# Performance work log

Measured on AMD Instinct MI355X. Metric: run time of the kernel, lower is better.

The kernel has to match this reference:

```python
import jax, jax.numpy as jnp
import numpy as np

B, N, F, S, M, K = 32, 4096, 256, 256, 1024, 11
EPS = 1e-06  # slot-attention epsilon
LN_EPS = 1e-05  # torch LayerNorm default
NUM_ITERS = 3


def _ln(x, g, b):
    mu = jnp.mean(x, axis=-1, keepdims=True)
    var = jnp.mean(jnp.square(x - mu), axis=-1, keepdims=True)
    return (x - mu) * jax.lax.rsqrt(var + LN_EPS) * g + b


def setup_inputs() -> dict:
    key = jax.random.key(0)
    ks = jax.random.split(key, 12)
    def xavier(k, shape):
        fan_in, fan_out = shape[0], shape[-1]
        lim = np.sqrt(6.0 / (fan_in + fan_out))
        return jax.random.uniform(k, shape, jnp.float32, -lim, lim)
    return {
        "features": jax.random.normal(ks[0], (B, N, F), jnp.float32),
        "sigma": jnp.array([0.1], jnp.float32),
        "z": jax.random.normal(ks[1], (B, K, S), jnp.float32),
        "slots_init_w": xavier(ks[2], (K, S)),
        "gf": jnp.ones((F,), jnp.float32), "bf": jnp.zeros((F,), jnp.float32),
        "gs": jnp.ones((S,), jnp.float32), "bs": jnp.zeros((S,), jnp.float32),
        "gm": jnp.ones((S,), jnp.float32), "bm": jnp.zeros((S,), jnp.float32),
        "Wk": xavier(ks[3], (F, S)),
        "Wv": xavier(ks[4], (F, S)),
        "Wq": xavier(ks[5], (S, S)),
        "W_ih": xavier(ks[6], (3 * S, S)),
        "W_hh": xavier(ks[7], (3 * S, S)),
        "b_ih": jnp.zeros((3 * S,), jnp.float32),
        "b_hh": jnp.zeros((3 * S,), jnp.float32),
        "W1": xavier(ks[8], (S, M)), "b1": jnp.zeros((M,), jnp.float32),
        "W2": xavier(ks[9], (M, S)), "b2": jnp.zeros((S,), jnp.float32),
    }


def _gru(x, h, W_ih, W_hh, b_ih, b_hh):
    # torch GRUCell: gates ordered (r, z, n)
    gi = x @ W_ih.T + b_ih  # [..., 3S]
    gh = h @ W_hh.T + b_hh
    ir, iz, inn = jnp.split(gi, 3, axis=-1)
    hr, hz, hn = jnp.split(gh, 3, axis=-1)
    r = jax.nn.sigmoid(ir + hr)
    zg = jax.nn.sigmoid(iz + hz)
    n = jnp.tanh(inn + r * hn)
    return (1.0 - zg) * n + zg * h


def reference(features, sigma, z, slots_init_w, gf, bf, gs, bs, gm, bm,
              Wk, Wv, Wq, W_ih, W_hh, b_ih, b_hh, W1, b1, W2, b2):
    mu = jnp.broadcast_to(slots_init_w[None], (features.shape[0], K, S))
    slots_init = mu + z * sigma * jax.lax.stop_gradient(mu)
    feats = _ln(features, gf, bf)
    k = feats @ Wk  # [B,N,S]
    v = feats @ Wv  # [B,N,S]
    D = v.shape[-1]
    scale = D ** -0.5
    slots = slots_init
    attn = None
    for i in range(NUM_ITERS):
        if i == NUM_ITERS - 1:
            slots = jax.lax.stop_gradient(slots) + slots_init - jax.lax.stop_gradient(slots_init)
        slots_prev = slots
        q = _ln(slots, gs, bs) @ Wq  # [B,K,S]
        attn_logits = jnp.einsum('bid,bjd->bij', q, k) * scale  # [B,K,N]
        attn = jax.nn.softmax(attn_logits, axis=1)  # softmax over slots axis
        attn_wm = attn / (jnp.sum(attn, axis=-1, keepdims=True) + EPS)
        updates = jnp.einsum('bij,bjd->bid', attn_wm, v)  # [B,K,S]
        slots = _gru(updates, slots_prev, W_ih, W_hh, b_ih, b_hh)
        slots = slots + (jax.nn.relu(_ln(slots, gm, bm) @ W1 + b1) @ W2 + b2)
    return slots, attn
```

## Files before the change

### kernel.cpp

```cpp
#include <hip/hip_runtime.h>

#define EPS 1e-6f
#define LN_EPS 1e-5f

typedef unsigned short u16;
typedef unsigned int u32;
typedef short bf16x8 __attribute__((ext_vector_type(8)));
typedef float f32x4 __attribute__((ext_vector_type(4)));

__device__ __forceinline__ float bf2f(u16 u) {
  return __uint_as_float(((u32)u) << 16);
}
__device__ __forceinline__ u16 f2bf(float f) {
  u32 x = __float_as_uint(f);
  x += 0x7fffu + ((x >> 16) & 1u);
  return (u16)(x >> 16);
}

__global__ void init_slots_kernel(const float* __restrict__ w,
                                  const float* __restrict__ z,
                                  const float* __restrict__ sigma,
                                  float* __restrict__ slots,
                                  float* __restrict__ upd,
                                  float* __restrict__ sums) {
  int i = blockIdx.x * 256 + threadIdx.x;
  int s = i & 255;
  int k = (i >> 8) % 11;
  float wv = w[k * 256 + s];
  slots[i] = wv + z[i] * sigma[0] * wv;
  upd[i] = 0.f;
  if (i < 352) sums[i] = 0.f;
}

__global__ void wprep_kernel(const float* __restrict__ W_ih,
                             const float* __restrict__ W_hh,
                             const float* __restrict__ W1,
                             const float* __restrict__ W2,
                             const float* __restrict__ Wq,
                             const float* __restrict__ Wk,
                             const float* __restrict__ Wv,
                             float* __restrict__ wihT, float* __restrict__ whhT,
                             short* __restrict__ W1b, short* __restrict__ W2b,
                             short* __restrict__ Wqb, short* __restrict__ Btb) {
  int e = blockIdx.x * 256 + threadIdx.x;
  if (e < 196608) {
    int j = e >> 8, d = e & 255;
    wihT[d * 768 + j] = W_ih[e];
  } else if (e < 393216) {
    int e2 = e - 196608;
    int j = e2 >> 8, d = e2 & 255;
    whhT[d * 768 + j] = W_hh[e2];
  } else if (e < 655360) {
    int e2 = e - 393216;
    W1b[e2] = (short)f2bf(W1[e2]);
  } else if (e < 917504) {
    int e2 = e - 655360;
    W2b[e2] = (short)f2bf(W2[e2]);
  } else if (e < 983040) {
    int e2 = e - 917504;
    Wqb[e2] = (short)f2bf(Wq[e2]);
  } else if (e < 1114112) {
    int e2 = e - 983040;
    int f = e2 >> 9, j = e2 & 511;
    float v = (j < 256) ? Wk[f * 256 + j] : Wv[f * 256 + (j - 256)];
    Btb[j * 256 + f] = (short)f2bf(v);
  }
}

__global__ __launch_bounds__(256) void gemm_kv(
    const float* __restrict__ feat, const short* __restrict__ Btb,
    const float* __restrict__ gf, const float* __restrict__ bfp,
    short* __restrict__ kt, short* __restrict__ vbuf) {
  __shared__ short As[16384];
  __shared__ short Bs[2][8192];
  int t = threadIdx.x;
  int w = t >> 6, lane = t & 63;
  int quad = lane >> 4, l16 = lane & 15;
  int i0 = blockIdx.x * 64;
  int wi = (w & 1) * 32, wj = (w >> 1) * 64;

  {
    #pragma unroll
    for (int c = 0; c < 4; ++c) {
      int lin = c * 256 + t;
      int jr = lin >> 3, p = lin & 7;
      int q = (p - jr) & 7;
      const short* gB = Btb + (long)jr * 256 + q * 8;
      __builtin_amdgcn_global_load_lds(
          (const __attribute__((address_space(1))) void*)gB,
          (__attribute__((address_space(3))) void*)&Bs[0][lin * 8], 16, 0, 0);
    }
  }

  {
    int r = t >> 2;
    int qd = t & 3;
    const float* frow = feat + (long)(i0 + r) * 256 + qd * 64;
    float4 fv[16];
    float s = 0.f, s2 = 0.f;
    #pragma unroll
    for (int i = 0; i < 16; ++i) {
      fv[i] = *(const float4*)(frow + i * 4);
      s += fv[i].x + fv[i].y + fv[i].z + fv[i].w;
      s2 += fv[i].x * fv[i].x + fv[i].y * fv[i].y + fv[i].z * fv[i].z +
            fv[i].w * fv[i].w;
    }
    s += __shfl_xor(s, 1); s2 += __shfl_xor(s2, 1);
    s += __shfl_xor(s, 2); s2 += __shfl_xor(s2, 2);
    float mu = s * (1.f / 256.f);
    float rs = rsqrtf(s2 * (1.f / 256.f) - mu * mu + LN_EPS);
    #pragma unroll
    for (int c = 0; c < 8; ++c) {
      float4 a = fv[c * 2], b = fv[c * 2 + 1];
      int fb = qd * 64 + c * 8;
      float4 g0 = *(const float4*)(gf + fb);
      float4 g1 = *(const float4*)(gf + fb + 4);
      float4 e0 = *(const float4*)(bfp + fb);
      float4 e1 = *(const float4*)(bfp + fb + 4);
      bf16x8 pk;
      pk[0] = (short)f2bf((a.x - mu) * rs * g0.x + e0.x);
      pk[1] = (short)f2bf((a.y - mu) * rs * g0.y + e0.y);
      pk[2] = (short)f2bf((a.z - mu) * rs * g0.z + e0.z);
      pk[3] = (short)f2bf((a.w - mu) * rs * g0.w + e0.w);
      pk[4] = (short)f2bf((b.x - mu) * rs * g1.x + e1.x);
      pk[5] = (short)f2bf((b.y - mu) * rs * g1.y + e1.y);
      pk[6] = (short)f2bf((b.z - mu) * rs * g1.z + e1.z);
      pk[7] = (short)f2bf((b.w - mu) * rs * g1.w + e1.w);
      int p = qd * 8 + ((c + 2 * qd + r) & 7);
      *(bf16x8*)&As[r * 256 + p * 8] = pk;
    }
  }
  __syncthreads();

  f32x4 acc[2][4];
  #pragma unroll
  for (int a = 0; a < 2; ++a)
    #pragma unroll
    for (int b = 0; b < 4; ++b) acc[a][b] = (f32x4){0.f, 0.f, 0.f, 0.f};

  for (int idx = 0; idx < 16; ++idx) {
    int jq = idx >> 2, ks = idx & 3;
    int buf = idx & 1;
    if (idx < 15) {
      int jn = (idx + 1) >> 2, kn = (idx + 1) & 3;
      #pragma unroll
      for (int c = 0; c < 4; ++c) {
        int lin = c * 256 + t;
        int jr = lin >> 3, p = lin & 7;
        int q = (p - jr) & 7;
        const short* gB = Btb + (long)(jn * 128 + jr) * 256 + kn * 64 + q * 8;
        __builtin_amdgcn_global_load_lds(
            (const __attribute__((address_space(1))) void*)gB,
            (__attribute__((address_space(3))) void*)&Bs[buf ^ 1][lin * 8],
            16, 0, 0);
      }
    }
    #pragma unroll
    for (int kh = 0; kh < 2; ++kh) {
      bf16x8 af[2], bfr[4];
      #pragma unroll
      for (int mi = 0; mi < 2; ++mi) {
        int m = wi + mi * 16 + l16;
        int p = ks * 8 + ((kh * 4 + quad + 2 * ks + m) & 7);
        af[mi] = *(const bf16x8*)&As[m * 256 + p * 8];
      }
      #pragma unroll
      for (int ni = 0; ni < 4; ++ni) {
        int j = wj + ni * 16 + l16;
        int p = ((kh * 4 + quad) + j) & 7;
        bfr[ni] = *(const bf16x8*)&Bs[buf][j * 64 + p * 8];
      }
      if (jq < 2) {
        #pragma unroll
        for (int mi = 0; mi < 2; ++mi)
          #pragma unroll
          for (int ni = 0; ni < 4; ++ni)
            acc[mi][ni] = __builtin_amdgcn_mfma_f32_16x16x32_bf16(
                af[mi], bfr[ni], acc[mi][ni], 0, 0, 0);
      } else {
        #pragma unroll
        for (int mi = 0; mi < 2; ++mi)
          #pragma unroll
          for (int ni = 0; ni < 4; ++ni)
            acc[mi][ni] = __builtin_amdgcn_mfma_f32_16x16x32_bf16(
                bfr[ni], af[mi], acc[mi][ni], 0, 0, 0);
      }
    }
    if (ks == 3) {
      if (jq < 2) {
        #pragma unroll
        for (int ni = 0; ni < 4; ++ni) {
          int j = jq * 128 + wj + ni * 16 + l16;
          #pragma unroll
          for (int mi = 0; mi < 2; ++mi) {
            long ib = i0 + wi + mi * 16 + quad * 4;
            ushort4 u;
            u.x = f2bf(acc[mi][ni][0]);
            u.y = f2bf(acc[mi][ni][1]);
            u.z = f2bf(acc[mi][ni][2]);
            u.w = f2bf(acc[mi][ni][3]);
            *(ushort4*)&kt[(long)j * 131072 + ib] = u;
          }
        }
      } else {
        #pragma unroll
        for (int mi = 0; mi < 2; ++mi) {
          long i = i0 + wi + mi * 16 + l16;
          #pragma unroll
          for (int ni = 0; ni < 4; ++ni) {
            int sb = (jq - 2) * 128 + wj + ni * 16 + quad * 4;
            ushort4 u;
            u.x = f2bf(acc[mi][ni][0]);
            u.y = f2bf(acc[mi][ni][1]);
            u.z = f2bf(acc[mi][ni][2]);
            u.w = f2bf(acc[mi][ni][3]);
            *(ushort4*)&vbuf[i * 256 + sb] = u;
          }
        }
      }
      #pragma unroll
      for (int a = 0; a < 2; ++a)
        #pragma unroll
        for (int b = 0; b < 4; ++b) acc[a][b] = (f32x4){0.f, 0.f, 0.f, 0.f};
    }
    __syncthreads();
  }
}

__global__ __launch_bounds__(256) void qproj_kernel(
    const float* __restrict__ slots, const float* __restrict__ gs,
    const float* __restrict__ bs, const short* __restrict__ Wqb,
    float* __restrict__ qout) {
  __shared__ float lnq[256];
  __shared__ float red[8];
  int row = blockIdx.x, t = threadIdx.x;
  int w = t >> 6, lane = t & 63;
  float x = slots[(long)row * 256 + t];
  float s = x, s2 = x * x;
  #pragma unroll
  for (int off = 32; off > 0; off >>= 1) {
    s += __shfl_xor(s, off);
    s2 += __shfl_xor(s2, off);
  }
  if (lane == 0) { red[w * 2] = s; red[w * 2 + 1] = s2; }
  __syncthreads();
  float st = red[0] + red[2] + red[4] + red[6];
  float st2 = red[1] + red[3] + red[5] + red[7];
  float mu = st * (1.f / 256.f);
  float rs = rsqrtf(st2 * (1.f / 256.f) - mu * mu + LN_EPS);
  lnq[t] = (x - mu) * rs * gs[t] + bs[t];
  __syncthreads();
  float acc = 0.f;
  for (int k = 0; k < 256; ++k)
    acc += lnq[k] * bf2f((u16)Wqb[k * 256 + t]);
  qout[(long)row * 256 + t] = acc;
}

__global__ __launch_bounds__(256) void attn_upd(
    const float* __restrict__ q, const short* __restrict__ kt,
    const short* __restrict__ vb, float* __restrict__ attn_out,
    float* __restrict__ sums, float* __restrict__ upd, int emit_attn) {
  __shared__ float qs[3072];
  __shared__ float ps[11 * 512];
  int b = blockIdx.y;
  int n0 = blockIdx.x * 512;
  int t = threadIdx.x, lane = t & 63;
  for (int e = t; e < 2816; e += 256) {
    int kk = e >> 8, f = e & 255;
    qs[f * 12 + kk] = q[b * 2816 + e];
  }
  __syncthreads();
  long base = (long)b * 4096 + n0 + 2 * t;
  float a0[11], a1[11];
  #pragma unroll
  for (int kk = 0; kk < 11; ++kk) { a0[kk] = 0.f; a1[kk] = 0.f; }
  for (int f = 0; f < 256; ++f) {
    u32 u = *(const u32*)(kt + (long)f * 131072 + base);
    float k0 = bf2f((u16)(u & 0xffffu));
    float k1 = bf2f((u16)(u >> 16));
    float4 qa = *(const float4*)&qs[f * 12];
    float4 qb4 = *(const float4*)&qs[f * 12 + 4];
    float4 qc = *(const float4*)&qs[f * 12 + 8];
    a0[0] += k0 * qa.x;  a1[0] += k1 * qa.x;
    a0[1] += k0 * qa.y;  a1[1] += k1 * qa.y;
    a0[2] += k0 * qa.z;  a1[2] += k1 * qa.z;
    a0[3] += k0 * qa.w;  a1[3] += k1 * qa.w;
    a0[4] += k0 * qb4.x; a1[4] += k1 * qb4.x;
    a0[5] += k0 * qb4.y; a1[5] += k1 * qb4.y;
    a0[6] += k0 * qb4.z; a1[6] += k1 * qb4.z;
    a0[7] += k0 * qb4.w; a1[7] += k1 * qb4.w;
    a0[8] += k0 * qc.x;  a1[8] += k1 * qc.x;
    a0[9] += k0 * qc.y;  a1[9] += k1 * qc.y;
    a0[10] += k0 * qc.z; a1[10] += k1 * qc.z;
  }
  float m0 = -1e30f, m1 = -1e30f;
  #pragma unroll
  for (int kk = 0; kk < 11; ++kk) {
    a0[kk] *= 0.0625f;
    a1[kk] *= 0.0625f;
    m0 = fmaxf(m0, a0[kk]);
    m1 = fmaxf(m1, a1[kk]);
  }
  float s0 = 0.f, s1 = 0.f;
  #pragma unroll
  for (int kk = 0; kk < 11; ++kk) {
    a0[kk] = expf(a0[kk] - m0);
    a1[kk] = expf(a1[kk] - m1);
    s0 += a0[kk];
    s1 += a1[kk];
  }
  float i0 = 1.0f / s0, i1 = 1.0f / s1;
  #pragma unroll
  for (int kk = 0; kk < 11; ++kk) {
    float p0 = a0[kk] * i0, p1 = a1[kk] * i1;
    *(float2*)&ps[kk * 512 + 2 * t] = make_float2(p0, p1);
    if (emit_attn)
      *(float2*)(attn_out + ((long)b * 11 + kk) * 4096 + n0 + 2 * t) =
          make_float2(p0, p1);
    float sv = p0 + p1;
    #pragma unroll
    for (int off = 32; off > 0; off >>= 1) sv += __shfl_xor(sv, off);
    if (lane == 0) atomicAdd(&sums[b * 11 + kk], sv);
  }
  __syncthreads();
  int sp = t & 127, nh = t >> 7;
  float2 acc[11];
  #pragma unroll
  for (int kk = 0; kk < 11; ++kk) acc[kk] = make_float2(0.f, 0.f);
  const u32* vb2 =
      (const u32*)(vb + ((long)b * 4096 + n0 + nh * 256) * 256);
  int pbase = nh * 256;
  for (int n4 = 0; n4 < 256; n4 += 4) {
    u32 u0 = vb2[(n4 + 0) * 128 + sp];
    u32 u1 = vb2[(n4 + 1) * 128 + sp];
    u32 u2 = vb2[(n4 + 2) * 128 + sp];
    u32 u3 = vb2[(n4 + 3) * 128 + sp];
    float v0x = bf2f((u16)(u0 & 0xffffu)), v0y = bf2f((u16)(u0 >> 16));
    float v1x = bf2f((u16)(u1 & 0xffffu)), v1y = bf2f((u16)(u1 >> 16));
    float v2x = bf2f((u16)(u2 & 0xffffu)), v2y = bf2f((u16)(u2 >> 16));
    float v3x = bf2f((u16)(u3 & 0xffffu)), v3y = bf2f((u16)(u3 >> 16));
    #pragma unroll
    for (int kk = 0; kk < 11; ++kk) {
      float4 a4 = *(const float4*)&ps[kk * 512 + pbase + n4];
      acc[kk].x += a4.x * v0x + a4.y * v1x + a4.z * v2x + a4.w * v3x;
      acc[kk].y += a4.x * v0y + a4.y * v1y + a4.z * v2y + a4.w * v3y;
    }
  }
  __syncthreads();
  if (nh == 1) {
    #pragma unroll
    for (int kk = 0; kk < 11; ++kk) {
      qs[kk * 256 + 2 * sp] = acc[kk].x;
      qs[kk * 256 + 2 * sp + 1] = acc[kk].y;
    }
  }
  __syncthreads();
  if (nh == 0) {
    #pragma unroll
    for (int kk = 0; kk < 11; ++kk) {
      atomicAdd(&upd[((long)b * 11 + kk) * 256 + 2 * sp],
                acc[kk].x + qs[kk * 256 + 2 * sp]);
      atomicAdd(&upd[((long)b * 11 + kk) * 256 + 2 * sp + 1],
                acc[kk].y + qs[kk * 256 + 2 * sp + 1]);
    }
  }
}

__global__ __launch_bounds__(256) void slot_step(
    float* __restrict__ upd, float* __restrict__ sums,
    const float* __restrict__ slots_in,
    const float* __restrict__ wihT, const float* __restrict__ whhT,
    const float* __restrict__ b_ih, const float* __restrict__ b_hh,
    const float* __restrict__ gm, const float* __restrict__ bm,
    const short* __restrict__ W1b, const float* __restrict__ b1,
    const short* __restrict__ W2b, const float* __restrict__ b2,
    const float* __restrict__ gs, const float* __restrict__ bs,
    const short* __restrict__ Wqb,
    float* __restrict__ slots_out, float* __restrict__ qout, int emit_q) {
  __shared__ float xs[2][256], hs[2][256], sgv[2][256], ln1[2][256];
  __shared__ float giv[2][768], ghv[2][768];
  __shared__ float h1v[2][1024];
  __shared__ float pw2[4][2][256];
  __shared__ float red[2][2];
  int t = threadIdx.x;
  int w = t >> 6, lane = t & 63;
  int r0 = blockIdx.x * 2;
  #pragma unroll
  for (int row = 0; row < 2; ++row) {
    int r = r0 + row;
    float sc = 1.0f / (sums[r] + EPS);
    xs[row][t] = upd[(long)r * 256 + t] * sc;
    hs[row][t] = slots_in[(long)r * 256 + t];
  }
  __syncthreads();
  #pragma unroll
  for (int row = 0; row < 2; ++row) {
    upd[(long)(r0 + row) * 256 + t] = 0.f;
    if (t == row) sums[r0 + row] = 0.f;
  }
  {
    float accI[2][3] = {}, accH[2][3] = {};
    for (int k = 0; k < 256; ++k) {
      float x0 = xs[0][k], x1 = xs[1][k];
      float h0 = hs[0][k], h1 = hs[1][k];
      #pragma unroll
      for (int j = 0; j < 3; ++j) {
        float wI = wihT[k * 768 + j * 256 + t];
        float wH = whhT[k * 768 + j * 256 + t];
        accI[0][j] += x0 * wI; accI[1][j] += x1 * wI;
        accH[0][j] += h0 * wH; accH[1][j] += h1 * wH;
      }
    }
    #pragma unroll
    for (int row = 0; row < 2; ++row)
      #pragma unroll
      for (int j = 0; j < 3; ++j) {
        giv[row][j * 256 + t] = accI[row][j] + b_ih[j * 256 + t];
        ghv[row][j * 256 + t] = accH[row][j] + b_hh[j * 256 + t];
      }
  }
  __syncthreads();
  #pragma unroll
  for (int row = 0; row < 2; ++row) {
    float irv = giv[row][t], izv = giv[row][256 + t], inv = giv[row][512 + t];
    float hrv = ghv[row][t], hzv = ghv[row][256 + t], hnv = ghv[row][512 + t];
    float hv = hs[row][t];
    float rg = 1.f / (1.f + expf(-(irv + hrv)));
    float zg = 1.f / (1.f + expf(-(izv + hzv)));
    float ng = tanhf(inv + rg * hnv);
    sgv[row][t] = (1.f - zg) * ng + zg * hv;
  }
  __syncthreads();
  if (w < 2) {
    float4 sv = *(const float4*)&sgv[w][lane * 4];
    float s = sv.x + sv.y + sv.z + sv.w;
    float s2 = sv.x * sv.x + sv.y * sv.y + sv.z * sv.z + sv.w * sv.w;
    #pragma unroll
    for (int off = 32; off > 0; off >>= 1) {
      s += __shfl_xor(s, off);
      s2 += __shfl_xor(s2, off);
    }
    if (lane == 0) {
      float mu = s * (1.f / 256.f);
      red[w][0] = mu;
      red[w][1] = rsqrtf(s2 * (1.f / 256.f) - mu * mu + LN_EPS);
    }
  }
  __syncthreads();
  #pragma unroll
  for (int row = 0; row < 2; ++row)
    ln1[row][t] = (sgv[row][t] - red[row][0]) * red[row][1] * gm[t] + bm[t];
  __syncthreads();
  {
    float acc1[2][4] = {};
    for (int k = 0; k < 256; ++k) {
      ushort4 w4 = *(const ushort4*)(W1b + (long)k * 1024 + 4 * t);
      float wv[4] = {bf2f(w4.x), bf2f(w4.y), bf2f(w4.z), bf2f(w4.w)};
      float l0 = ln1[0][k], l1 = ln1[1][k];
      #pragma unroll
      for (int j = 0; j < 4; ++j) {
        acc1[0][j] += l0 * wv[j];
        acc1[1][j] += l1 * wv[j];
      }
    }
    #pragma unroll
    for (int row = 0; row < 2; ++row)
      #pragma unroll
      for (int j = 0; j < 4; ++j)
        h1v[row][4 * t + j] = fmaxf(acc1[row][j] + b1[4 * t + j], 0.f);
  }
  __syncthreads();
  {
    float acc2[2][4] = {};
    int kbase = w * 256;
    for (int kk = 0; kk < 256; ++kk) {
      int k = kbase + kk;
      ushort4 w4 = *(const ushort4*)(W2b + (long)k * 256 + 4 * lane);
      float wv[4] = {bf2f(w4.x), bf2f(w4.y), bf2f(w4.z), bf2f(w4.w)};
      float h0 = h1v[0][k], h1 = h1v[1][k];
      #pragma unroll
      for (int j = 0; j < 4; ++j) {
        acc2[0][j] += h0 * wv[j];
        acc2[1][j] += h1 * wv[j];
      }
    }
    #pragma unroll
    for (int row = 0; row < 2; ++row)
      #pragma unroll
      for (int j = 0; j < 4; ++j) pw2[w][row][4 * lane + j] = acc2[row][j];
  }
  __syncthreads();
  float outv[2];
  #pragma unroll
  for (int row = 0; row < 2; ++row) {
    float s = pw2[0][row][t] + pw2[1][row][t] + pw2[2][row][t] + pw2[3][row][t];
    outv[row] = s + b2[t] + sgv[row][t];
    slots_out[(long)(r0 + row) * 256 + t] = outv[row];
  }
  if (emit_q) {
    __syncthreads();
    xs[0][t] = outv[0];
    xs[1][t] = outv[1];
    __syncthreads();
    if (w < 2) {
      float4 sv = *(const float4*)&xs[w][lane * 4];
      float s = sv.x + sv.y + sv.z + sv.w;
      float s2 = sv.x * sv.x + sv.y * sv.y + sv.z * sv.z + sv.w * sv.w;
      #pragma unroll
      for (int off = 32; off > 0; off >>= 1) {
        s += __shfl_xor(s, off);
        s2 += __shfl_xor(s2, off);
      }
      if (lane == 0) {
        float mu = s * (1.f / 256.f);
        red[w][0] = mu;
        red[w][1] = rsqrtf(s2 * (1.f / 256.f) - mu * mu + LN_EPS);
      }
    }
    __syncthreads();
    #pragma unroll
    for (int row = 0; row < 2; ++row)
      hs[row][t] = (xs[row][t] - red[row][0]) * red[row][1] * gs[t] + bs[t];
    __syncthreads();
    float accq[2] = {};
    for (int k = 0; k < 256; ++k) {
      float wq = bf2f((u16)Wqb[k * 256 + t]);
      accq[0] += hs[0][k] * wq;
      accq[1] += hs[1][k] * wq;
    }
    #pragma unroll
    for (int row = 0; row < 2; ++row)
      qout[(long)(r0 + row) * 256 + t] = accq[row];
  }
}

extern "C" void kernel_launch(void* const* d_in, const int* in_sizes, int n_in,
                              void* d_out, int out_size, void* d_ws,
                              size_t ws_size, hipStream_t stream) {
  const float* features = (const float*)d_in[0];
  const float* sigma = (const float*)d_in[1];
  const float* z = (const float*)d_in[2];
  const float* slots_init_w = (const float*)d_in[3];
  const float* gf = (const float*)d_in[4];
  const float* bf = (const float*)d_in[5];
  const float* gs = (const float*)d_in[6];
  const float* bs = (const float*)d_in[7];
  const float* gm = (const float*)d_in[8];
  const float* bm = (const float*)d_in[9];
  const float* Wk = (const float*)d_in[10];
  const float* Wv = (const float*)d_in[11];
  const float* Wq = (const float*)d_in[12];
  const float* W_ih = (const float*)d_in[13];
  const float* W_hh = (const float*)d_in[14];
  const float* b_ih = (const float*)d_in[15];
  const float* b_hh = (const float*)d_in[16];
  const float* W1 = (const float*)d_in[17];
  const float* b1 = (const float*)d_in[18];
  const float* W2 = (const float*)d_in[19];
  const float* b2 = (const float*)d_in[20];

  float* ws = (float*)d_ws;
  size_t o = 0;
  short* ktb = (short*)(ws + o); o += 16777216;
  short* vbuf = (short*)(ws + o); o += 16777216;
  short* Btb = (short*)(ws + o); o += 65536;
  float* wihT = ws + o; o += 196608;
  float* whhT = ws + o; o += 196608;
  short* W1b = (short*)(ws + o); o += 131072;
  short* W2b = (short*)(ws + o); o += 131072;
  short* Wqb = (short*)(ws + o); o += 32768;
  float* slots = ws + o; o += 90112;
  float* qbuf = ws + o; o += 90112;
  float* upd = ws + o; o += 90112;
  float* sums = ws + o; o += 352;

  float* out_slots = (float*)d_out;
  float* out_attn = (float*)d_out + 90112;

  init_slots_kernel<<<352, 256, 0, stream>>>(slots_init_w, z, sigma, slots,
                                             upd, sums);
  wprep_kernel<<<4352, 256, 0, stream>>>(W_ih, W_hh, W1, W2, Wq, Wk, Wv,
                                         wihT, whhT, W1b, W2b, Wqb, Btb);
  gemm_kv<<<2048, 256, 0, stream>>>(features, Btb, gf, bf, ktb, vbuf);
  qproj_kernel<<<352, 256, 0, stream>>>(slots, gs, bs, Wqb, qbuf);

  for (int it = 0; it < 3; ++it) {
    attn_upd<<<dim3(8, 32), 256, 0, stream>>>(
        qbuf, ktb, vbuf, out_attn, sums, upd, (it == 2) ? 1 : 0);
    slot_step<<<176, 256, 0, stream>>>(
        upd, sums, slots, wihT, whhT, b_ih, b_hh, gm, bm, W1b, b1, W2b, b2,
        gs, bs, Wqb, (it == 2) ? out_slots : slots, qbuf, (it < 2) ? 1 : 0);
  }
}
```

Measured before the change: 775.4 us.

## Store V transposed and compute attention-weighted updates with MFMA

The K/V projection kernel now writes both K and V in a transposed [feature][token] layout into one buffer and reads B operands straight from global memory instead of double-buffering them through LDS. The attention kernel processes 256 tokens per block (twice as many blocks), stores bf16 probabilities in LDS, and computes the attn·V update with 16x16x32 bf16 MFMA instead of scalar FMA loops. The aim is to move the update reduction onto matrix cores and simplify the GEMM. In exchange, probabilities are rounded to bf16 before the update, 11 of 16 MFMA rows do useful work, and the GEMM loses LDS staging for B, which may raise global/L2 traffic.

```diff
diff --git a/kernel.cpp b/kernel.cpp
--- a/kernel.cpp
+++ b/kernel.cpp
@@ -70,27 +70,13 @@
 __global__ __launch_bounds__(256) void gemm_kv(
     const float* __restrict__ feat, const short* __restrict__ Btb,
     const float* __restrict__ gf, const float* __restrict__ bfp,
-    short* __restrict__ kt, short* __restrict__ vbuf) {
+    short* __restrict__ ktv) {
   __shared__ short As[16384];
-  __shared__ short Bs[2][8192];
   int t = threadIdx.x;
   int w = t >> 6, lane = t & 63;
   int quad = lane >> 4, l16 = lane & 15;
   int i0 = blockIdx.x * 64;
   int wi = (w & 1) * 32, wj = (w >> 1) * 64;
-
-  {
-    #pragma unroll
-    for (int c = 0; c < 4; ++c) {
-      int lin = c * 256 + t;
-      int jr = lin >> 3, p = lin & 7;
-      int q = (p - jr) & 7;
-      const short* gB = Btb + (long)jr * 256 + q * 8;
-      __builtin_amdgcn_global_load_lds(
-          (const __attribute__((address_space(1))) void*)gB,
-          (__attribute__((address_space(3))) void*)&Bs[0][lin * 8], 16, 0, 0);
-    }
-  }
 
   {
     int r = t >> 2;
@@ -132,98 +118,50 @@
   }
   __syncthreads();
 
-  f32x4 acc[2][4];
-  #pragma unroll
-  for (int a = 0; a < 2; ++a)
-    #pragma unroll
-    for (int b = 0; b < 4; ++b) acc[a][b] = (f32x4){0.f, 0.f, 0.f, 0.f};
-
-  for (int idx = 0; idx < 16; ++idx) {
-    int jq = idx >> 2, ks = idx & 3;
-    int buf = idx & 1;
-    if (idx < 15) {
-      int jn = (idx + 1) >> 2, kn = (idx + 1) & 3;
-      #pragma unroll
-      for (int c = 0; c < 4; ++c) {
-        int lin = c * 256 + t;
-        int jr = lin >> 3, p = lin & 7;
-        int q = (p - jr) & 7;
-        const short* gB = Btb + (long)(jn * 128 + jr) * 256 + kn * 64 + q * 8;
-        __builtin_amdgcn_global_load_lds(
-            (const __attribute__((address_space(1))) void*)gB,
-            (__attribute__((address_space(3))) void*)&Bs[buf ^ 1][lin * 8],
-            16, 0, 0);
-      }
-    }
-    #pragma unroll
-    for (int kh = 0; kh < 2; ++kh) {
-      bf16x8 af[2], bfr[4];
-      #pragma unroll
-      for (int mi = 0; mi < 2; ++mi) {
-        int m = wi + mi * 16 + l16;
-        int p = ks * 8 + ((kh * 4 + quad + 2 * ks + m) & 7);
-        af[mi] = *(const bf16x8*)&As[m * 256 + p * 8];
-      }
-      #pragma unroll
-      for (int ni = 0; ni < 4; ++ni) {
-        int j = wj + ni * 16 + l16;
-        int p = ((kh * 4 + quad) + j) & 7;
-        bfr[ni] = *(const bf16x8*)&Bs[buf][j * 64 + p * 8];
-      }
-      if (jq < 2) {
+  const short* bb = Btb + (long)(wj + l16) * 256 + quad * 8;
+  for (int jq = 0; jq < 4; ++jq) {
+    f32x4 acc[2][4];
+    #pragma unroll
+    for (int a = 0; a < 2; ++a)
+      #pragma unroll
+      for (int b = 0; b < 4; ++b) acc[a][b] = (f32x4){0.f, 0.f, 0.f, 0.f};
+    #pragma unroll
+    for (int ks = 0; ks < 4; ++ks) {
+      #pragma unroll
+      for (int kh = 0; kh < 2; ++kh) {
+        int koff = ks * 64 + kh * 32;
+        bf16x8 af[2], bfr[4];
+        #pragma unroll
+        for (int mi = 0; mi < 2; ++mi) {
+          int m = wi + mi * 16 + l16;
+          int p = ks * 8 + ((kh * 4 + quad + 2 * ks + m) & 7);
+          af[mi] = *(const bf16x8*)&As[m * 256 + p * 8];
+        }
+        #pragma unroll
+        for (int ni = 0; ni < 4; ++ni)
+          bfr[ni] = *(const bf16x8*)&bb[(long)(jq * 128 + ni * 16) * 256 + koff];
         #pragma unroll
         for (int mi = 0; mi < 2; ++mi)
           #pragma unroll
           for (int ni = 0; ni < 4; ++ni)
             acc[mi][ni] = __builtin_amdgcn_mfma_f32_16x16x32_bf16(
                 af[mi], bfr[ni], acc[mi][ni], 0, 0, 0);
-      } else {
-        #pragma unroll
-        for (int mi = 0; mi < 2; ++mi)
-          #pragma unroll
-          for (int ni = 0; ni < 4; ++ni)
-            acc[mi][ni] = __builtin_amdgcn_mfma_f32_16x16x32_bf16(
-                bfr[ni], af[mi], acc[mi][ni], 0, 0, 0);
-      }
-    }
-    if (ks == 3) {
-      if (jq < 2) {
-        #pragma unroll
-        for (int ni = 0; ni < 4; ++ni) {
-          int j = jq * 128 + wj + ni * 16 + l16;
-          #pragma unroll
-          for (int mi = 0; mi < 2; ++mi) {
-            long ib = i0 + wi + mi * 16 + quad * 4;
-            ushort4 u;
-            u.x = f2bf(acc[mi][ni][0]);
-            u.y = f2bf(acc[mi][ni][1]);
-            u.z = f2bf(acc[mi][ni][2]);
-            u.w = f2bf(acc[mi][ni][3]);
-            *(ushort4*)&kt[(long)j * 131072 + ib] = u;
-          }
-        }
-      } else {
-        #pragma unroll
-        for (int mi = 0; mi < 2; ++mi) {
-          long i = i0 + wi + mi * 16 + l16;
-          #pragma unroll
-          for (int ni = 0; ni < 4; ++ni) {
-            int sb = (jq - 2) * 128 + wj + ni * 16 + quad * 4;
-            ushort4 u;
-            u.x = f2bf(acc[mi][ni][0]);
-            u.y = f2bf(acc[mi][ni][1]);
-            u.z = f2bf(acc[mi][ni][2]);
-            u.w = f2bf(acc[mi][ni][3]);
-            *(ushort4*)&vbuf[i * 256 + sb] = u;
-          }
-        }
-      }
-      #pragma unroll
-      for (int a = 0; a < 2; ++a)
-        #pragma unroll
-        for (int b = 0; b < 4; ++b) acc[a][b] = (f32x4){0.f, 0.f, 0.f, 0.f};
-    }
-    __syncthreads();
+      }
+    }
+    #pragma unroll
+    for (int ni = 0; ni < 4; ++ni) {
+      int j = jq * 128 + wj + ni * 16 + l16;
+      #pragma unroll
+      for (int mi = 0; mi < 2; ++mi) {
+        long ib = i0 + wi + mi * 16 + quad * 4;
+        ushort4 u;
+        u.x = f2bf(acc[mi][ni][0]);
+        u.y = f2bf(acc[mi][ni][1]);
+        u.z = f2bf(acc[mi][ni][2]);
+        u.w = f2bf(acc[mi][ni][3]);
+        *(ushort4*)&ktv[(long)j * 131072 + ib] = u;
+      }
+    }
   }
 }
 
@@ -257,111 +195,85 @@
 }
 
 __global__ __launch_bounds__(256) void attn_upd(
-    const float* __restrict__ q, const short* __restrict__ kt,
-    const short* __restrict__ vb, float* __restrict__ attn_out,
-    float* __restrict__ sums, float* __restrict__ upd, int emit_attn) {
+    const float* __restrict__ q, const short* __restrict__ ktv,
+    float* __restrict__ attn_out, float* __restrict__ sums,
+    float* __restrict__ upd, int emit_attn) {
   __shared__ float qs[3072];
-  __shared__ float ps[11 * 512];
+  __shared__ short ps[16 * 264];
   int b = blockIdx.y;
-  int n0 = blockIdx.x * 512;
+  int n0 = blockIdx.x * 256;
   int t = threadIdx.x, lane = t & 63;
+  int w = t >> 6, quad = lane >> 4, l16 = lane & 15;
   for (int e = t; e < 2816; e += 256) {
     int kk = e >> 8, f = e & 255;
     qs[f * 12 + kk] = q[b * 2816 + e];
   }
-  __syncthreads();
-  long base = (long)b * 4096 + n0 + 2 * t;
-  float a0[11], a1[11];
-  #pragma unroll
-  for (int kk = 0; kk < 11; ++kk) { a0[kk] = 0.f; a1[kk] = 0.f; }
+  for (int e = t; e < 5 * 264; e += 256) ps[11 * 264 + e] = 0;
+  __syncthreads();
+  long bn = (long)b * 4096 + n0 + t;
+  float a[11];
+  #pragma unroll
+  for (int kk = 0; kk < 11; ++kk) a[kk] = 0.f;
   for (int f = 0; f < 256; ++f) {
-    u32 u = *(const u32*)(kt + (long)f * 131072 + base);
-    float k0 = bf2f((u16)(u & 0xffffu));
-    float k1 = bf2f((u16)(u >> 16));
+    float kv = bf2f((u16)ktv[(long)f * 131072 + bn]);
     float4 qa = *(const float4*)&qs[f * 12];
     float4 qb4 = *(const float4*)&qs[f * 12 + 4];
     float4 qc = *(const float4*)&qs[f * 12 + 8];
-    a0[0] += k0 * qa.x;  a1[0] += k1 * qa.x;
-    a0[1] += k0 * qa.y;  a1[1] += k1 * qa.y;
-    a0[2] += k0 * qa.z;  a1[2] += k1 * qa.z;
-    a0[3] += k0 * qa.w;  a1[3] += k1 * qa.w;
-    a0[4] += k0 * qb4.x; a1[4] += k1 * qb4.x;
-    a0[5] += k0 * qb4.y; a1[5] += k1 * qb4.y;
-    a0[6] += k0 * qb4.z; a1[6] += k1 * qb4.z;
-    a0[7] += k0 * qb4.w; a1[7] += k1 * qb4.w;
-    a0[8] += k0 * qc.x;  a1[8] += k1 * qc.x;
-    a0[9] += k0 * qc.y;  a1[9] += k1 * qc.y;
-    a0[10] += k0 * qc.z; a1[10] += k1 * qc.z;
-  }
-  float m0 = -1e30f, m1 = -1e30f;
+    a[0] += kv * qa.x;  a[1] += kv * qa.y;  a[2] += kv * qa.z;
+    a[3] += kv * qa.w;  a[4] += kv * qb4.x; a[5] += kv * qb4.y;
+    a[6] += kv * qb4.z; a[7] += kv * qb4.w; a[8] += kv * qc.x;
+    a[9] += kv * qc.y;  a[10] += kv * qc.z;
+  }
+  float mx = -1e30f;
   #pragma unroll
   for (int kk = 0; kk < 11; ++kk) {
-    a0[kk] *= 0.0625f;
-    a1[kk] *= 0.0625f;
-    m0 = fmaxf(m0, a0[kk]);
-    m1 = fmaxf(m1, a1[kk]);
-  }
-  float s0 = 0.f, s1 = 0.f;
+    a[kk] *= 0.0625f;
+    mx = fmaxf(mx, a[kk]);
+  }
+  float ssum = 0.f;
   #pragma unroll
   for (int kk = 0; kk < 11; ++kk) {
-    a0[kk] = expf(a0[kk] - m0);
-    a1[kk] = expf(a1[kk] - m1);
-    s0 += a0[kk];
-    s1 += a1[kk];
-  }
-  float i0 = 1.0f / s0, i1 = 1.0f / s1;
+    a[kk] = expf(a[kk] - mx);
+    ssum += a[kk];
+  }
+  float inv = 1.0f / ssum;
   #pragma unroll
   for (int kk = 0; kk < 11; ++kk) {
-    float p0 = a0[kk] * i0, p1 = a1[kk] * i1;
-    *(float2*)&ps[kk * 512 + 2 * t] = make_float2(p0, p1);
-    if (emit_attn)
-      *(float2*)(attn_out + ((long)b * 11 + kk) * 4096 + n0 + 2 * t) =
-          make_float2(p0, p1);
-    float sv = p0 + p1;
+    float p = a[kk] * inv;
+    a[kk] = p;
+    ps[kk * 264 + t] = (short)f2bf(p);
+    if (emit_attn) attn_out[((long)b * 11 + kk) * 4096 + n0 + t] = p;
+  }
+  #pragma unroll
+  for (int kk = 0; kk < 11; ++kk) {
+    float sv = a[kk];
     #pragma unroll
     for (int off = 32; off > 0; off >>= 1) sv += __shfl_xor(sv, off);
     if (lane == 0) atomicAdd(&sums[b * 11 + kk], sv);
   }
   __syncthreads();
-  int sp = t & 127, nh = t >> 7;
-  float2 acc[11];
-  #pragma unroll
-  for (int kk = 0; kk < 11; ++kk) acc[kk] = make_float2(0.f, 0.f);
-  const u32* vb2 =
-      (const u32*)(vb + ((long)b * 4096 + n0 + nh * 256) * 256);
-  int pbase = nh * 256;
-  for (int n4 = 0; n4 < 256; n4 += 4) {
-    u32 u0 = vb2[(n4 + 0) * 128 + sp];
-    u32 u1 = vb2[(n4 + 1) * 128 + sp];
-    u32 u2 = vb2[(n4 + 2) * 128 + sp];
-    u32 u3 = vb2[(n4 + 3) * 128 + sp];
-    float v0x = bf2f((u16)(u0 & 0xffffu)), v0y = bf2f((u16)(u0 >> 16));
-    float v1x = bf2f((u16)(u1 & 0xffffu)), v1y = bf2f((u16)(u1 >> 16));
-    float v2x = bf2f((u16)(u2 & 0xffffu)), v2y = bf2f((u16)(u2 >> 16));
-    float v3x = bf2f((u16)(u3 & 0xffffu)), v3y = bf2f((u16)(u3 >> 16));
-    #pragma unroll
-    for (int kk = 0; kk < 11; ++kk) {
-      float4 a4 = *(const float4*)&ps[kk * 512 + pbase + n4];
-      acc[kk].x += a4.x * v0x + a4.y * v1x + a4.z * v2x + a4.w * v3x;
-      acc[kk].y += a4.x * v0y + a4.y * v1y + a4.z * v2y + a4.w * v3y;
-    }
-  }
-  __syncthreads();
-  if (nh == 1) {
-    #pragma unroll
-    for (int kk = 0; kk < 11; ++kk) {
-      qs[kk * 256 + 2 * sp] = acc[kk].x;
-      qs[kk * 256 + 2 * sp + 1] = acc[kk].y;
-    }
-  }
-  __syncthreads();
-  if (nh == 0) {
-    #pragma unroll
-    for (int kk = 0; kk < 11; ++kk) {
-      atomicAdd(&upd[((long)b * 11 + kk) * 256 + 2 * sp],
-                acc[kk].x + qs[kk * 256 + 2 * sp]);
-      atomicAdd(&upd[((long)b * 11 + kk) * 256 + 2 * sp + 1],
-                acc[kk].y + qs[kk * 256 + 2 * sp + 1]);
+  const short* vT = ktv + (long)256 * 131072;
+  f32x4 acc[4];
+  #pragma unroll
+  for (int mi = 0; mi < 4; ++mi) acc[mi] = (f32x4){0.f, 0.f, 0.f, 0.f};
+  #pragma unroll
+  for (int kst = 0; kst < 8; ++kst) {
+    int nb = kst * 32 + quad * 8;
+    bf16x8 bps = *(const bf16x8*)&ps[l16 * 264 + nb];
+    #pragma unroll
+    for (int mi = 0; mi < 4; ++mi) {
+      int s = (w * 4 + mi) * 16 + l16;
+      bf16x8 av = *(const bf16x8*)&vT[(long)s * 131072 + (long)b * 4096 + n0 + nb];
+      acc[mi] = __builtin_amdgcn_mfma_f32_16x16x32_bf16(av, bps, acc[mi], 0, 0, 0);
+    }
+  }
+  if (l16 < 11) {
+    #pragma unroll
+    for (int mi = 0; mi < 4; ++mi) {
+      int sb = (w * 4 + mi) * 16 + quad * 4;
+      #pragma unroll
+      for (int r = 0; r < 4; ++r)
+        atomicAdd(&upd[((long)b * 11 + l16) * 256 + sb + r], acc[mi][r]);
     }
   }
 }
@@ -561,8 +473,7 @@
 
   float* ws = (float*)d_ws;
   size_t o = 0;
-  short* ktb = (short*)(ws + o); o += 16777216;
-  short* vbuf = (short*)(ws + o); o += 16777216;
+  short* ktv = (short*)(ws + o); o += 33554432;
   short* Btb = (short*)(ws + o); o += 65536;
   float* wihT = ws + o; o += 196608;
   float* whhT = ws + o; o += 196608;
@@ -581,12 +492,12 @@
                                              upd, sums);
   wprep_kernel<<<4352, 256, 0, stream>>>(W_ih, W_hh, W1, W2, Wq, Wk, Wv,
                                          wihT, whhT, W1b, W2b, Wqb, Btb);
-  gemm_kv<<<2048, 256, 0, stream>>>(features, Btb, gf, bf, ktb, vbuf);
+  gemm_kv<<<2048, 256, 0, stream>>>(features, Btb, gf, bf, ktv);
   qproj_kernel<<<352, 256, 0, stream>>>(slots, gs, bs, Wqb, qbuf);
 
   for (int it = 0; it < 3; ++it) {
-    attn_upd<<<dim3(8, 32), 256, 0, stream>>>(
-        qbuf, ktb, vbuf, out_attn, sums, upd, (it == 2) ? 1 : 0);
+    attn_upd<<<dim3(16, 32), 256, 0, stream>>>(
+        qbuf, ktv, out_attn, sums, upd, (it == 2) ? 1 : 0);
     slot_step<<<176, 256, 0, stream>>>(
         upd, sums, slots, wihT, whhT, b_ih, b_hh, gm, bm, W1b, b1, W2b, b2,
         gs, bs, Wqb, (it == 2) ? out_slots : slots, qbuf, (it < 2) ? 1 : 0);
```

Result: slower. 876.9 us (+13.1%).

## Use MFMA for attention logits and updates, swap K/V output layouts

Applied to the files above, without the earlier changes.

The attention kernel's scalar FP32 dot products for q·k and attn·v are replaced with bf16 MFMA instructions, with q and the probabilities staged in LDS as bf16. The KV GEMM now writes k row-major and v transposed so both MFMA operand loads are contiguous. The slot-init kernel is merged into the weight-prep kernel, removing one launch. In exchange, q and the attention probabilities are rounded to bf16 before the update matmul, and the 11 slots are padded to 16 MFMA columns, which wastes part of each instruction.

```diff
diff --git a/kernel.cpp b/kernel.cpp
--- a/kernel.cpp
+++ b/kernel.cpp
@@ -17,31 +17,21 @@
   return (u16)(x >> 16);
 }
 
-__global__ void init_slots_kernel(const float* __restrict__ w,
-                                  const float* __restrict__ z,
-                                  const float* __restrict__ sigma,
-                                  float* __restrict__ slots,
-                                  float* __restrict__ upd,
-                                  float* __restrict__ sums) {
-  int i = blockIdx.x * 256 + threadIdx.x;
-  int s = i & 255;
-  int k = (i >> 8) % 11;
-  float wv = w[k * 256 + s];
-  slots[i] = wv + z[i] * sigma[0] * wv;
-  upd[i] = 0.f;
-  if (i < 352) sums[i] = 0.f;
-}
-
-__global__ void wprep_kernel(const float* __restrict__ W_ih,
-                             const float* __restrict__ W_hh,
-                             const float* __restrict__ W1,
-                             const float* __restrict__ W2,
-                             const float* __restrict__ Wq,
-                             const float* __restrict__ Wk,
-                             const float* __restrict__ Wv,
-                             float* __restrict__ wihT, float* __restrict__ whhT,
-                             short* __restrict__ W1b, short* __restrict__ W2b,
-                             short* __restrict__ Wqb, short* __restrict__ Btb) {
+__global__ void prep_kernel(const float* __restrict__ W_ih,
+                            const float* __restrict__ W_hh,
+                            const float* __restrict__ W1,
+                            const float* __restrict__ W2,
+                            const float* __restrict__ Wq,
+                            const float* __restrict__ Wk,
+                            const float* __restrict__ Wv,
+                            const float* __restrict__ slots_init_w,
+                            const float* __restrict__ z,
+                            const float* __restrict__ sigma,
+                            float* __restrict__ wihT, float* __restrict__ whhT,
+                            short* __restrict__ W1b, short* __restrict__ W2b,
+                            short* __restrict__ Wqb, short* __restrict__ Btb,
+                            float* __restrict__ slots, float* __restrict__ upd,
+                            float* __restrict__ sums) {
   int e = blockIdx.x * 256 + threadIdx.x;
   if (e < 196608) {
     int j = e >> 8, d = e & 255;
@@ -64,13 +54,21 @@
     int f = e2 >> 9, j = e2 & 511;
     float v = (j < 256) ? Wk[f * 256 + j] : Wv[f * 256 + (j - 256)];
     Btb[j * 256 + f] = (short)f2bf(v);
+  } else if (e < 1204224) {
+    int i = e - 1114112;
+    int s = i & 255;
+    int k = (i >> 8) % 11;
+    float wv = slots_init_w[k * 256 + s];
+    slots[i] = wv + z[i] * sigma[0] * wv;
+    upd[i] = 0.f;
+    if (i < 352) sums[i] = 0.f;
   }
 }
 
 __global__ __launch_bounds__(256) void gemm_kv(
     const float* __restrict__ feat, const short* __restrict__ Btb,
     const float* __restrict__ gf, const float* __restrict__ bfp,
-    short* __restrict__ kt, short* __restrict__ vbuf) {
+    short* __restrict__ knorm, short* __restrict__ vT) {
   __shared__ short As[16384];
   __shared__ short Bs[2][8192];
   int t = threadIdx.x;
@@ -176,21 +174,36 @@
           #pragma unroll
           for (int ni = 0; ni < 4; ++ni)
             acc[mi][ni] = __builtin_amdgcn_mfma_f32_16x16x32_bf16(
-                af[mi], bfr[ni], acc[mi][ni], 0, 0, 0);
+                bfr[ni], af[mi], acc[mi][ni], 0, 0, 0);
       } else {
         #pragma unroll
         for (int mi = 0; mi < 2; ++mi)
           #pragma unroll
           for (int ni = 0; ni < 4; ++ni)
             acc[mi][ni] = __builtin_amdgcn_mfma_f32_16x16x32_bf16(
-                bfr[ni], af[mi], acc[mi][ni], 0, 0, 0);
+                af[mi], bfr[ni], acc[mi][ni], 0, 0, 0);
       }
     }
     if (ks == 3) {
       if (jq < 2) {
         #pragma unroll
+        for (int mi = 0; mi < 2; ++mi) {
+          long i = i0 + wi + mi * 16 + l16;
+          #pragma unroll
+          for (int ni = 0; ni < 4; ++ni) {
+            int fb = jq * 128 + wj + ni * 16 + quad * 4;
+            ushort4 u;
+            u.x = f2bf(acc[mi][ni][0]);
+            u.y = f2bf(acc[mi][ni][1]);
+            u.z = f2bf(acc[mi][ni][2]);
+            u.w = f2bf(acc[mi][ni][3]);
+            *(ushort4*)&knorm[i * 256 + fb] = u;
+          }
+        }
+      } else {
+        #pragma unroll
         for (int ni = 0; ni < 4; ++ni) {
-          int j = jq * 128 + wj + ni * 16 + l16;
+          int s = (jq - 2) * 128 + wj + ni * 16 + l16;
           #pragma unroll
           for (int mi = 0; mi < 2; ++mi) {
             long ib = i0 + wi + mi * 16 + quad * 4;
@@ -199,22 +212,7 @@
             u.y = f2bf(acc[mi][ni][1]);
             u.z = f2bf(acc[mi][ni][2]);
             u.w = f2bf(acc[mi][ni][3]);
-            *(ushort4*)&kt[(long)j * 131072 + ib] = u;
-          }
-        }
-      } else {
-        #pragma unroll
-        for (int mi = 0; mi < 2; ++mi) {
-          long i = i0 + wi + mi * 16 + l16;
-          #pragma unroll
-          for (int ni = 0; ni < 4; ++ni) {
-            int sb = (jq - 2) * 128 + wj + ni * 16 + quad * 4;
-            ushort4 u;
-            u.x = f2bf(acc[mi][ni][0]);
-            u.y = f2bf(acc[mi][ni][1]);
-            u.z = f2bf(acc[mi][ni][2]);
-            u.w = f2bf(acc[mi][ni][3]);
-            *(ushort4*)&vbuf[i * 256 + sb] = u;
+            *(ushort4*)&vT[(long)s * 131072 + ib] = u;
           }
         }
       }
@@ -257,111 +255,90 @@
 }
 
 __global__ __launch_bounds__(256) void attn_upd(
-    const float* __restrict__ q, const short* __restrict__ kt,
-    const short* __restrict__ vb, float* __restrict__ attn_out,
+    const float* __restrict__ q, const short* __restrict__ knorm,
+    const short* __restrict__ vT, float* __restrict__ attn_out,
     float* __restrict__ sums, float* __restrict__ upd, int emit_attn) {
-  __shared__ float qs[3072];
-  __shared__ float ps[11 * 512];
+  __shared__ short qs[16 * 264];
+  __shared__ short ps[16 * 520];
   int b = blockIdx.y;
   int n0 = blockIdx.x * 512;
   int t = threadIdx.x, lane = t & 63;
+  int w = t >> 6, quad = lane >> 4, l16 = lane & 15;
+  for (int e = t; e < 5 * 264; e += 256) qs[11 * 264 + e] = 0;
   for (int e = t; e < 2816; e += 256) {
     int kk = e >> 8, f = e & 255;
-    qs[f * 12 + kk] = q[b * 2816 + e];
-  }
-  __syncthreads();
-  long base = (long)b * 4096 + n0 + 2 * t;
-  float a0[11], a1[11];
-  #pragma unroll
-  for (int kk = 0; kk < 11; ++kk) { a0[kk] = 0.f; a1[kk] = 0.f; }
-  for (int f = 0; f < 256; ++f) {
-    u32 u = *(const u32*)(kt + (long)f * 131072 + base);
-    float k0 = bf2f((u16)(u & 0xffffu));
-    float k1 = bf2f((u16)(u >> 16));
-    float4 qa = *(const float4*)&qs[f * 12];
-    float4 qb4 = *(const float4*)&qs[f * 12 + 4];
-    float4 qc = *(const float4*)&qs[f * 12 + 8];
-    a0[0] += k0 * qa.x;  a1[0] += k1 * qa.x;
-    a0[1] += k0 * qa.y;  a1[1] += k1 * qa.y;
-    a0[2] += k0 * qa.z;  a1[2] += k1 * qa.z;
-    a0[3] += k0 * qa.w;  a1[3] += k1 * qa.w;
-    a0[4] += k0 * qb4.x; a1[4] += k1 * qb4.x;
-    a0[5] += k0 * qb4.y; a1[5] += k1 * qb4.y;
-    a0[6] += k0 * qb4.z; a1[6] += k1 * qb4.z;
-    a0[7] += k0 * qb4.w; a1[7] += k1 * qb4.w;
-    a0[8] += k0 * qc.x;  a1[8] += k1 * qc.x;
-    a0[9] += k0 * qc.y;  a1[9] += k1 * qc.y;
-    a0[10] += k0 * qc.z; a1[10] += k1 * qc.z;
-  }
-  float m0 = -1e30f, m1 = -1e30f;
-  #pragma unroll
-  for (int kk = 0; kk < 11; ++kk) {
-    a0[kk] *= 0.0625f;
-    a1[kk] *= 0.0625f;
-    m0 = fmaxf(m0, a0[kk]);
-    m1 = fmaxf(m1, a1[kk]);
-  }
-  float s0 = 0.f, s1 = 0.f;
-  #pragma unroll
-  for (int kk = 0; kk < 11; ++kk) {
-    a0[kk] = expf(a0[kk] - m0);
-    a1[kk] = expf(a1[kk] - m1);
-    s0 += a0[kk];
-    s1 += a1[kk];
-  }
-  float i0 = 1.0f / s0, i1 = 1.0f / s1;
-  #pragma unroll
-  for (int kk = 0; kk < 11; ++kk) {
-    float p0 = a0[kk] * i0, p1 = a1[kk] * i1;
-    *(float2*)&ps[kk * 512 + 2 * t] = make_float2(p0, p1);
-    if (emit_attn)
-      *(float2*)(attn_out + ((long)b * 11 + kk) * 4096 + n0 + 2 * t) =
-          make_float2(p0, p1);
-    float sv = p0 + p1;
-    #pragma unroll
-    for (int off = 32; off > 0; off >>= 1) sv += __shfl_xor(sv, off);
-    if (lane == 0) atomicAdd(&sums[b * 11 + kk], sv);
-  }
-  __syncthreads();
-  int sp = t & 127, nh = t >> 7;
-  float2 acc[11];
-  #pragma unroll
-  for (int kk = 0; kk < 11; ++kk) acc[kk] = make_float2(0.f, 0.f);
-  const u32* vb2 =
-      (const u32*)(vb + ((long)b * 4096 + n0 + nh * 256) * 256);
-  int pbase = nh * 256;
-  for (int n4 = 0; n4 < 256; n4 += 4) {
-    u32 u0 = vb2[(n4 + 0) * 128 + sp];
-    u32 u1 = vb2[(n4 + 1) * 128 + sp];
-    u32 u2 = vb2[(n4 + 2) * 128 + sp];
-    u32 u3 = vb2[(n4 + 3) * 128 + sp];
-    float v0x = bf2f((u16)(u0 & 0xffffu)), v0y = bf2f((u16)(u0 >> 16));
-    float v1x = bf2f((u16)(u1 & 0xffffu)), v1y = bf2f((u16)(u1 >> 16));
-    float v2x = bf2f((u16)(u2 & 0xffffu)), v2y = bf2f((u16)(u2 >> 16));
-    float v3x = bf2f((u16)(u3 & 0xffffu)), v3y = bf2f((u16)(u3 >> 16));
-    #pragma unroll
-    for (int kk = 0; kk < 11; ++kk) {
-      float4 a4 = *(const float4*)&ps[kk * 512 + pbase + n4];
-      acc[kk].x += a4.x * v0x + a4.y * v1x + a4.z * v2x + a4.w * v3x;
-      acc[kk].y += a4.x * v0y + a4.y * v1y + a4.z * v2y + a4.w * v3y;
-    }
-  }
-  __syncthreads();
-  if (nh == 1) {
-    #pragma unroll
-    for (int kk = 0; kk < 11; ++kk) {
-      qs[kk * 256 + 2 * sp] = acc[kk].x;
-      qs[kk * 256 + 2 * sp + 1] = acc[kk].y;
-    }
-  }
-  __syncthreads();
-  if (nh == 0) {
-    #pragma unroll
-    for (int kk = 0; kk < 11; ++kk) {
-      atomicAdd(&upd[((long)b * 11 + kk) * 256 + 2 * sp],
-                acc[kk].x + qs[kk * 256 + 2 * sp]);
-      atomicAdd(&upd[((long)b * 11 + kk) * 256 + 2 * sp + 1],
-                acc[kk].y + qs[kk * 256 + 2 * sp + 1]);
+    qs[kk * 264 + f] = (short)f2bf(q[b * 2816 + e]);
+  }
+  __syncthreads();
+  f32x4 acc[8];
+  #pragma unroll
+  for (int mi = 0; mi < 8; ++mi) acc[mi] = (f32x4){0.f, 0.f, 0.f, 0.f};
+  long nbase = (long)b * 4096 + n0 + w * 128;
+  const short* kb = knorm + (nbase + l16) * 256 + quad * 8;
+  #pragma unroll
+  for (int c = 0; c < 8; ++c) {
+    bf16x8 qf = *(const bf16x8*)&qs[l16 * 264 + c * 32 + quad * 8];
+    #pragma unroll
+    for (int mi = 0; mi < 8; ++mi) {
+      bf16x8 kf = *(const bf16x8*)&kb[mi * 16 * 256 + c * 32];
+      acc[mi] = __builtin_amdgcn_mfma_f32_16x16x32_bf16(kf, qf, acc[mi], 0, 0, 0);
+    }
+  }
+  bool valid = l16 < 11;
+  float slsum = 0.f;
+  #pragma unroll
+  for (int mi = 0; mi < 8; ++mi) {
+    float4 pv;
+    #pragma unroll
+    for (int r = 0; r < 4; ++r) {
+      float L = acc[mi][r] * 0.0625f;
+      float Lm = valid ? L : -1e30f;
+      Lm = fmaxf(Lm, __shfl_xor(Lm, 1));
+      Lm = fmaxf(Lm, __shfl_xor(Lm, 2));
+      Lm = fmaxf(Lm, __shfl_xor(Lm, 4));
+      Lm = fmaxf(Lm, __shfl_xor(Lm, 8));
+      float p = valid ? expf(L - Lm) : 0.f;
+      float ss = p;
+      ss += __shfl_xor(ss, 1);
+      ss += __shfl_xor(ss, 2);
+      ss += __shfl_xor(ss, 4);
+      ss += __shfl_xor(ss, 8);
+      p = p / ss;
+      (&pv.x)[r] = p;
+      slsum += p;
+      ps[l16 * 520 + w * 128 + mi * 16 + quad * 4 + r] = (short)f2bf(p);
+    }
+    if (emit_attn && valid)
+      *(float4*)(attn_out + ((long)b * 11 + l16) * 4096 + n0 + w * 128 +
+                 mi * 16 + quad * 4) = pv;
+  }
+  slsum += __shfl_xor(slsum, 16);
+  slsum += __shfl_xor(slsum, 32);
+  if (valid && quad == 0) atomicAdd(&sums[b * 11 + l16], slsum);
+  __syncthreads();
+  f32x4 acc4[4];
+  #pragma unroll
+  for (int mi = 0; mi < 4; ++mi) acc4[mi] = (f32x4){0.f, 0.f, 0.f, 0.f};
+  #pragma unroll
+  for (int kst = 0; kst < 16; ++kst) {
+    int nb = kst * 32 + quad * 8;
+    bf16x8 bps = *(const bf16x8*)&ps[l16 * 520 + nb];
+    #pragma unroll
+    for (int mi = 0; mi < 4; ++mi) {
+      int s = (w * 4 + mi) * 16 + l16;
+      bf16x8 av =
+          *(const bf16x8*)&vT[(long)s * 131072 + (long)b * 4096 + n0 + nb];
+      acc4[mi] =
+          __builtin_amdgcn_mfma_f32_16x16x32_bf16(av, bps, acc4[mi], 0, 0, 0);
+    }
+  }
+  if (l16 < 11) {
+    #pragma unroll
+    for (int mi = 0; mi < 4; ++mi) {
+      int sb = (w * 4 + mi) * 16 + quad * 4;
+      #pragma unroll
+      for (int r = 0; r < 4; ++r)
+        atomicAdd(&upd[((long)b * 11 + l16) * 256 + sb + r], acc4[mi][r]);
     }
   }
 }
@@ -561,8 +538,8 @@
 
   float* ws = (float*)d_ws;
   size_t o = 0;
-  short* ktb = (short*)(ws + o); o += 16777216;
-  short* vbuf = (short*)(ws + o); o += 16777216;
+  short* knorm = (short*)(ws + o); o += 16777216;
+  short* vT = (short*)(ws + o); o += 16777216;
   short* Btb = (short*)(ws + o); o += 65536;
   float* wihT = ws + o; o += 196608;
   float* whhT = ws + o; o += 196608;
@@ -577,16 +554,15 @@
   float* out_slots = (float*)d_out;
   float* out_attn = (float*)d_out + 90112;
 
-  init_slots_kernel<<<352, 256, 0, stream>>>(slots_init_w, z, sigma, slots,
-                                             upd, sums);
-  wprep_kernel<<<4352, 256, 0, stream>>>(W_ih, W_hh, W1, W2, Wq, Wk, Wv,
-                                         wihT, whhT, W1b, W2b, Wqb, Btb);
-  gemm_kv<<<2048, 256, 0, stream>>>(features, Btb, gf, bf, ktb, vbuf);
+  prep_kernel<<<4704, 256, 0, stream>>>(W_ih, W_hh, W1, W2, Wq, Wk, Wv,
+                                        slots_init_w, z, sigma, wihT, whhT,
+                                        W1b, W2b, Wqb, Btb, slots, upd, sums);
+  gemm_kv<<<2048, 256, 0, stream>>>(features, Btb, gf, bf, knorm, vT);
   qproj_kernel<<<352, 256, 0, stream>>>(slots, gs, bs, Wqb, qbuf);
 
   for (int it = 0; it < 3; ++it) {
     attn_upd<<<dim3(8, 32), 256, 0, stream>>>(
-        qbuf, ktb, vbuf, out_attn, sums, upd, (it == 2) ? 1 : 0);
+        qbuf, knorm, vT, out_attn, sums, upd, (it == 2) ? 1 : 0);
     slot_step<<<176, 256, 0, stream>>>(
         upd, sums, slots, wihT, whhT, b_ih, b_hh, gm, bm, W1b, b1, W2b, b2,
         gs, bs, Wqb, (it == 2) ? out_slots : slots, qbuf, (it < 2) ? 1 : 0);
```

After: 689.1 us. -11.1%, faster.
